# Optimization experiments

Hardware: AMD Instinct MI355X
Metric: run time of the kernel (lower is better)

Reference implementation:

```python
import jax, jax.numpy as jnp
import numpy as np

TAO = 1.0
EPS = 1e-8


def setup_inputs() -> dict:
    key = jax.random.key(0)
    k1, k2, k3 = jax.random.split(key, 3)
    B, S, H = 32, 64, 256
    tmap = jax.random.normal(k1, (B, S, S, H), dtype=jnp.float32)
    pos_query = jax.random.normal(k2, (B, H), dtype=jnp.float32)
    r = jax.random.uniform(k3, (B, S, S))
    mask2d_pos = r < 0.05
    mask2d_neg = (r >= 0.05) & (r < 0.35)
    return {"pos_query": pos_query, "tmap": tmap,
            "mask2d_pos": mask2d_pos, "mask2d_neg": mask2d_neg}


def reference(pos_query, tmap, mask2d_pos, mask2d_neg):
    # Original loops over batch, gathers variable-length pos/neg sets, normalizes
    # twice (once without eps, once with eps inside sim()), then InfoNCE-style loss.
    # Vectorized: compute similarities for ALL (i,j) cells once, reduce with masks.
    u = tmap / jnp.linalg.norm(tmap, axis=-1, keepdims=True)          # pos/neg normalize (no eps)
    u = u / (jnp.linalg.norm(u, axis=-1, keepdims=True) + EPS)        # renormalize inside sim() (with eps)
    q = pos_query / (jnp.linalg.norm(pos_query, axis=-1, keepdims=True) + EPS)
    s = jnp.einsum('bijh,bh->bij', u, q)                              # cosine sims (B,S,S)
    e = jnp.exp(s / TAO)
    num = jnp.sum(e * mask2d_pos, axis=(1, 2))                        # sum exp(pos_sim/tao)
    den = num + jnp.sum(e * mask2d_neg, axis=(1, 2))                  # + sum exp(neg_sim/tao)
    li = -jnp.log(num / (den + EPS))                                  # per-sample loss (B,)
    # original skips samples with empty pos or neg set, averages over the rest
    valid = jnp.any(mask2d_pos, axis=(1, 2)) & jnp.any(mask2d_neg, axis=(1, 2))
    n_valid = jnp.maximum(jnp.sum(valid), 1)
    return jnp.sum(jnp.where(valid, li, 0.0)) / n_valid
```

## Files before the change

### kernel.cpp

```cpp
#include <hip/hip_runtime.h>
#include <math.h>

#define EPSF 1e-8f
constexpr int B = 32;
constexpr int S = 64;
constexpr int H = 256;
constexpr int H4 = H / 4;
constexpr int CELLS_PER_BATCH = S * S;
constexpr int CELLS = B * CELLS_PER_BATCH;
constexpr int CELLS_PER_WAVE = 8;
constexpr int WAVES_PER_BLOCK = 4;
constexpr int CELLS_PER_BLOCK = CELLS_PER_WAVE * WAVES_PER_BLOCK;

#define WS_ACC_BASE 64
#define WS_ACC_STRIDE 32
#define WS_NEG_OFF 16

__global__ __launch_bounds__(64) void prep_kernel(const float* __restrict__ pq,
                                                  float* __restrict__ ws) {
    int b = blockIdx.x;
    int lane = threadIdx.x;
    float4 v = ((const float4*)pq)[b * H4 + lane];
    float ss = v.x * v.x + v.y * v.y + v.z * v.z + v.w * v.w;
    #pragma unroll
    for (int off = 32; off > 0; off >>= 1) ss += __shfl_xor(ss, off);
    if (lane == 0) {
        ws[b] = 1.0f / (sqrtf(ss) + EPSF);
        ws[WS_ACC_BASE + b * WS_ACC_STRIDE] = 0.0f;
        ws[WS_ACC_BASE + b * WS_ACC_STRIDE + WS_NEG_OFF] = 0.0f;
    }
}

__global__ __launch_bounds__(256) void main_kernel(const float* __restrict__ tmap,
                                                   const float* __restrict__ pq,
                                                   const int* __restrict__ mask_pos,
                                                   const int* __restrict__ mask_neg,
                                                   float* __restrict__ ws) {
    int tid = threadIdx.x;
    int lane = tid & 63;
    int wid = tid >> 6;
    int cellBase = blockIdx.x * CELLS_PER_BLOCK + wid * CELLS_PER_WAVE;
    int b = cellBase >> 12;

    float4 q4 = ((const float4*)pq)[b * H4 + lane];
    float scale = ws[b] * (1.0f / (1.0f + EPSF));

    float wp = 0.0f, wn = 0.0f;
    #pragma unroll
    for (int k = 0; k < CELLS_PER_WAVE; ++k) {
        int cell = cellBase + k;
        float4 t = ((const float4*)tmap)[cell * H4 + lane];
        float d  = t.x * q4.x + t.y * q4.y + t.z * q4.z + t.w * q4.w;
        float ss = t.x * t.x + t.y * t.y + t.z * t.z + t.w * t.w;
        #pragma unroll
        for (int off = 32; off > 0; off >>= 1) {
            d  += __shfl_xor(d, off);
            ss += __shfl_xor(ss, off);
        }
        float s = d * scale * rsqrtf(ss);
        float e = __expf(s);
        if (mask_pos[cell] != 0) wp += e;
        if (mask_neg[cell] != 0) wn += e;
    }

    __shared__ float sp[WAVES_PER_BLOCK], sn[WAVES_PER_BLOCK];
    if (lane == 0) { sp[wid] = wp; sn[wid] = wn; }
    __syncthreads();
    if (tid == 0) {
        float tp = 0.0f, tn = 0.0f;
        #pragma unroll
        for (int w = 0; w < WAVES_PER_BLOCK; ++w) { tp += sp[w]; tn += sn[w]; }
        atomicAdd(&ws[WS_ACC_BASE + b * WS_ACC_STRIDE], tp);
        atomicAdd(&ws[WS_ACC_BASE + b * WS_ACC_STRIDE + WS_NEG_OFF], tn);
    }
}

__global__ __launch_bounds__(64) void final_kernel(const float* __restrict__ ws,
                                                   float* __restrict__ out) {
    int lane = threadIdx.x;
    float li = 0.0f;
    int v = 0;
    if (lane < B) {
        float ep = ws[WS_ACC_BASE + lane * WS_ACC_STRIDE];
        float en = ws[WS_ACC_BASE + lane * WS_ACC_STRIDE + WS_NEG_OFF];
        if (ep > 0.0f && en > 0.0f) {
            v = 1;
            li = -logf(ep / (ep + en + EPSF));
        }
    }
    #pragma unroll
    for (int off = 32; off > 0; off >>= 1) {
        li += __shfl_xor(li, off);
        v  += __shfl_xor(v, off);
    }
    if (lane == 0) out[0] = li / (float)(v > 0 ? v : 1);
}

extern "C" void kernel_launch(void* const* d_in, const int* in_sizes, int n_in,
                              void* d_out, int out_size, void* d_ws, size_t ws_size,
                              hipStream_t stream) {
    const float* pos_query = (const float*)d_in[0];
    const float* tmap      = (const float*)d_in[1];
    const int*   mask_pos  = (const int*)d_in[2];
    const int*   mask_neg  = (const int*)d_in[3];
    float* out = (float*)d_out;
    float* ws  = (float*)d_ws;

    prep_kernel<<<B, 64, 0, stream>>>(pos_query, ws);
    main_kernel<<<CELLS / CELLS_PER_BLOCK, 256, 0, stream>>>(tmap, pos_query,
                                                             mask_pos, mask_neg, ws);
    final_kernel<<<1, 64, 0, stream>>>(ws, out);
}
```

Before: 195.8 us.

## Skip unmasked cells, fold query norm into main kernel, drop atomics

The main kernel now reads the pos/neg masks first, builds ballot bitmasks, and loads tmap rows only for cells that are in one of the two masks. Roughly 65% of cells in neither set are skipped, which cuts HBM traffic substantially. It also processes four cells per wave at once with 16-lane groups, computes the query norm inline so the prep kernel is no longer needed, and replaces the per-batch atomics with per-block partial stores that a wider final kernel reduces. In exchange the memory accesses become data-dependent and gathered, and control flow diverges.

```diff
diff --git a/kernel.cpp b/kernel.cpp
--- a/kernel.cpp
+++ b/kernel.cpp
@@ -8,28 +8,12 @@
 constexpr int H4 = H / 4;
 constexpr int CELLS_PER_BATCH = S * S;
 constexpr int CELLS = B * CELLS_PER_BATCH;
-constexpr int CELLS_PER_WAVE = 8;
+constexpr int CELLS_PER_WAVE = 32;
 constexpr int WAVES_PER_BLOCK = 4;
 constexpr int CELLS_PER_BLOCK = CELLS_PER_WAVE * WAVES_PER_BLOCK;
+constexpr int BLOCKS_PER_BATCH = CELLS_PER_BATCH / CELLS_PER_BLOCK;
+constexpr int GRID = CELLS / CELLS_PER_BLOCK;
 
-#define WS_ACC_BASE 64
-#define WS_ACC_STRIDE 32
-#define WS_NEG_OFF 16
-
-__global__ __launch_bounds__(64) void prep_kernel(const float* __restrict__ pq,
-                                                  float* __restrict__ ws) {
-    int b = blockIdx.x;
-    int lane = threadIdx.x;
-    float4 v = ((const float4*)pq)[b * H4 + lane];
-    float ss = v.x * v.x + v.y * v.y + v.z * v.z + v.w * v.w;
-    #pragma unroll
-    for (int off = 32; off > 0; off >>= 1) ss += __shfl_xor(ss, off);
-    if (lane == 0) {
-        ws[b] = 1.0f / (sqrtf(ss) + EPSF);
-        ws[WS_ACC_BASE + b * WS_ACC_STRIDE] = 0.0f;
-        ws[WS_ACC_BASE + b * WS_ACC_STRIDE + WS_NEG_OFF] = 0.0f;
-    }
-}
 
 __global__ __launch_bounds__(256) void main_kernel(const float* __restrict__ tmap,
                                                    const float* __restrict__ pq,
@@ -39,61 +23,114 @@
     int tid = threadIdx.x;
     int lane = tid & 63;
     int wid = tid >> 6;
-    int cellBase = blockIdx.x * CELLS_PER_BLOCK + wid * CELLS_PER_WAVE;
-    int b = cellBase >> 12;
+    int b   = blockIdx.x >> 5;
+    int sub = blockIdx.x & 31;
+    int waveBase = blockIdx.x * CELLS_PER_BLOCK + wid * CELLS_PER_WAVE;
 
-    float4 q4 = ((const float4*)pq)[b * H4 + lane];
-    float scale = ws[b] * (1.0f / (1.0f + EPSF));
+    int p = lane & 15;
+    int g = lane >> 4;
 
+    const float4* q4 = (const float4*)pq + (size_t)b * H4;
+    float4 qm0 = q4[p], qm1 = q4[p + 16], qm2 = q4[p + 32], qm3 = q4[p + 48];
+
+    float ssq = qm0.x*qm0.x + qm0.y*qm0.y + qm0.z*qm0.z + qm0.w*qm0.w
+              + qm1.x*qm1.x + qm1.y*qm1.y + qm1.z*qm1.z + qm1.w*qm1.w
+              + qm2.x*qm2.x + qm2.y*qm2.y + qm2.z*qm2.z + qm2.w*qm2.w
+              + qm3.x*qm3.x + qm3.y*qm3.y + qm3.z*qm3.z + qm3.w*qm3.w;
+    #pragma unroll
+    for (int off = 1; off <= 8; off <<= 1) ssq += __shfl_xor(ssq, off);
+    float scale = (1.0f / (sqrtf(ssq) + EPSF)) * (1.0f / (1.0f + EPSF));
+
+    int mp = 0, mn = 0;
+    if (lane < CELLS_PER_WAVE) {
+        mp = mask_pos[waveBase + lane];
+        mn = mask_neg[waveBase + lane];
+    }
+    unsigned bp = (unsigned)__ballot(mp != 0);
+    unsigned bn = (unsigned)__ballot(mn != 0);
+    unsigned rem = bp | bn;
+
+    const float4* t4 = (const float4*)tmap;
     float wp = 0.0f, wn = 0.0f;
-    #pragma unroll
-    for (int k = 0; k < CELLS_PER_WAVE; ++k) {
-        int cell = cellBase + k;
-        float4 t = ((const float4*)tmap)[cell * H4 + lane];
-        float d  = t.x * q4.x + t.y * q4.y + t.z * q4.z + t.w * q4.w;
-        float ss = t.x * t.x + t.y * t.y + t.z * t.z + t.w * t.w;
-        #pragma unroll
-        for (int off = 32; off > 0; off >>= 1) {
-            d  += __shfl_xor(d, off);
-            ss += __shfl_xor(ss, off);
+
+    while (rem) {
+        int k0 = __ffs(rem) - 1; rem &= rem - 1;
+        int k1 = -1, k2 = -1, k3 = -1;
+        if (rem) { k1 = __ffs(rem) - 1; rem &= rem - 1;
+            if (rem) { k2 = __ffs(rem) - 1; rem &= rem - 1;
+                if (rem) { k3 = __ffs(rem) - 1; rem &= rem - 1; } } }
+        int kg = (g == 0) ? k0 : (g == 1) ? k1 : (g == 2) ? k2 : k3;
+        if (kg >= 0) {
+            const float4* cp = t4 + (size_t)(waveBase + kg) * H4 + p;
+            float4 t0 = cp[0], t1 = cp[16], t2 = cp[32], t3 = cp[48];
+            float d  = t0.x*qm0.x + t0.y*qm0.y + t0.z*qm0.z + t0.w*qm0.w
+                     + t1.x*qm1.x + t1.y*qm1.y + t1.z*qm1.z + t1.w*qm1.w
+                     + t2.x*qm2.x + t2.y*qm2.y + t2.z*qm2.z + t2.w*qm2.w
+                     + t3.x*qm3.x + t3.y*qm3.y + t3.z*qm3.z + t3.w*qm3.w;
+            float ss = t0.x*t0.x + t0.y*t0.y + t0.z*t0.z + t0.w*t0.w
+                     + t1.x*t1.x + t1.y*t1.y + t1.z*t1.z + t1.w*t1.w
+                     + t2.x*t2.x + t2.y*t2.y + t2.z*t2.z + t2.w*t2.w
+                     + t3.x*t3.x + t3.y*t3.y + t3.z*t3.z + t3.w*t3.w;
+            #pragma unroll
+            for (int off = 1; off <= 8; off <<= 1) {
+                d  += __shfl_xor(d, off);
+                ss += __shfl_xor(ss, off);
+            }
+            float s = d * scale * rsqrtf(ss);
+            float e = __expf(s);
+            if ((bp >> kg) & 1) wp += e;
+            if ((bn >> kg) & 1) wn += e;
         }
-        float s = d * scale * rsqrtf(ss);
-        float e = __expf(s);
-        if (mask_pos[cell] != 0) wp += e;
-        if (mask_neg[cell] != 0) wn += e;
     }
+
+    wp += __shfl_xor(wp, 16); wp += __shfl_xor(wp, 32);
+    wn += __shfl_xor(wn, 16); wn += __shfl_xor(wn, 32);
 
     __shared__ float sp[WAVES_PER_BLOCK], sn[WAVES_PER_BLOCK];
     if (lane == 0) { sp[wid] = wp; sn[wid] = wn; }
     __syncthreads();
     if (tid == 0) {
-        float tp = 0.0f, tn = 0.0f;
-        #pragma unroll
-        for (int w = 0; w < WAVES_PER_BLOCK; ++w) { tp += sp[w]; tn += sn[w]; }
-        atomicAdd(&ws[WS_ACC_BASE + b * WS_ACC_STRIDE], tp);
-        atomicAdd(&ws[WS_ACC_BASE + b * WS_ACC_STRIDE + WS_NEG_OFF], tn);
+        float tp = sp[0] + sp[1] + sp[2] + sp[3];
+        float tn = sn[0] + sn[1] + sn[2] + sn[3];
+        ((float2*)ws)[sub * B + b] = make_float2(tp, tn);
     }
 }
 
-__global__ __launch_bounds__(64) void final_kernel(const float* __restrict__ ws,
-                                                   float* __restrict__ out) {
-    int lane = threadIdx.x;
-    float li = 0.0f;
-    int v = 0;
-    if (lane < B) {
-        float ep = ws[WS_ACC_BASE + lane * WS_ACC_STRIDE];
-        float en = ws[WS_ACC_BASE + lane * WS_ACC_STRIDE + WS_NEG_OFF];
-        if (ep > 0.0f && en > 0.0f) {
-            v = 1;
-            li = -logf(ep / (ep + en + EPSF));
-        }
+__global__ __launch_bounds__(256) void final_kernel(const float* __restrict__ ws,
+                                                    float* __restrict__ out) {
+    const float2* pp = (const float2*)ws;
+    int tid = threadIdx.x;
+    int lane = tid & 63, w = tid >> 6;
+    int b = w * 8 + (lane >> 3);
+    int h = lane & 7;
+    float ep = 0.0f, en = 0.0f;
+    #pragma unroll
+    for (int m = 0; m < 4; ++m) {
+        float2 v = pp[(h + 8 * m) * B + b];
+        ep += v.x; en += v.y;
     }
     #pragma unroll
-    for (int off = 32; off > 0; off >>= 1) {
-        li += __shfl_xor(li, off);
-        v  += __shfl_xor(v, off);
+    for (int off = 1; off <= 4; off <<= 1) {
+        ep += __shfl_xor(ep, off);
+        en += __shfl_xor(en, off);
     }
-    if (lane == 0) out[0] = li / (float)(v > 0 ? v : 1);
+    __shared__ float2 acc[B];
+    if (h == 0) acc[b] = make_float2(ep, en);
+    __syncthreads();
+    if (tid < B) {
+        float2 a = acc[tid];
+        float li = 0.0f; int v = 0;
+        if (a.x > 0.0f && a.y > 0.0f) {
+            v = 1;
+            li = -logf(a.x / (a.x + a.y + EPSF));
+        }
+        #pragma unroll
+        for (int off = 16; off > 0; off >>= 1) {
+            li += __shfl_xor(li, off);
+            v  += __shfl_xor(v, off);
+        }
+        if (tid == 0) out[0] = li / (float)(v > 0 ? v : 1);
+    }
 }
 
 extern "C" void kernel_launch(void* const* d_in, const int* in_sizes, int n_in,
@@ -106,8 +143,6 @@
     float* out = (float*)d_out;
     float* ws  = (float*)d_ws;
 
-    prep_kernel<<<B, 64, 0, stream>>>(pos_query, ws);
-    main_kernel<<<CELLS / CELLS_PER_BLOCK, 256, 0, stream>>>(tmap, pos_query,
-                                                             mask_pos, mask_neg, ws);
-    final_kernel<<<1, 64, 0, stream>>>(ws, out);
+    main_kernel<<<GRID, 256, 0, stream>>>(tmap, pos_query, mask_pos, mask_neg, ws);
+    final_kernel<<<1, 256, 0, stream>>>(ws, out);
 }
```

Result: faster. 184.7 us (-5.6%).
